# Kernel optimization log

Hardware: AMD Instinct MI355X
Metric: run time of the kernel (lower is better)

## Reference

```python
import jax, jax.numpy as jnp
import numpy as np

N_HEAD = 16
N_EMBD = 1024
BLOCK = 2048
B, T = 4, 2048


def setup_inputs() -> dict:
    key = jax.random.key(0)
    ks = jax.random.split(key, 5)
    s = 0.02
    return {
        "x": jax.random.normal(ks[0], (B, T, N_EMBD), dtype=jnp.float32),
        "qkv_w": jax.random.normal(ks[1], (3 * N_EMBD, N_EMBD), dtype=jnp.float32) * s,
        "qkv_b": jnp.zeros((3 * N_EMBD,), dtype=jnp.float32),
        "proj_w": jax.random.normal(ks[2], (N_EMBD, N_EMBD), dtype=jnp.float32) * s,
        "proj_b": jnp.zeros((N_EMBD,), dtype=jnp.float32),
    }


def reference(x, qkv_w, qkv_b, proj_w, proj_b):
    Bx, Tx, C = x.shape
    hd = C // N_HEAD
    qkv = x @ qkv_w.T + qkv_b  # [B,T,3C]
    q, k, v = jnp.split(qkv, 3, axis=-1)
    # [B,T,C] -> [B,H,T,hd]
    def heads(t):
        return t.reshape(Bx, Tx, N_HEAD, hd).transpose(0, 2, 1, 3)
    q, k, v = heads(q), heads(k), heads(v)
    scores = jnp.einsum("bhqd,bhkd->bhqk", q, k) / jnp.sqrt(jnp.float32(hd))
    causal = jnp.tril(jnp.ones((Tx, Tx), dtype=bool))
    scores = jnp.where(causal[None, None, :, :], scores, -jnp.inf)
    attn = jax.nn.softmax(scores, axis=-1)
    out = jnp.einsum("bhqk,bhkd->bhqd", attn, v)
    out = out.transpose(0, 2, 1, 3).reshape(Bx, Tx, C)
    return out @ proj_w.T + proj_b
```

## Files before the change

kernel.cpp:

```cpp
#include <hip/hip_runtime.h>
#include <stdint.h>
#include <math.h>

#define DEVI __device__ __forceinline__

typedef __attribute__((ext_vector_type(8))) short bf16x8;
typedef __attribute__((ext_vector_type(4))) float f32x4;

DEVI unsigned short f2bf(float f) {
  union { float f; unsigned u; } v; v.f = f;
  unsigned u = v.u;
  u += 0x7fffu + ((u >> 16) & 1u);
  return (unsigned short)(u >> 16);
}

DEVI unsigned cvt_pk_bf16(float a, float b) {
  unsigned r;
  asm("v_cvt_pk_bf16_f32 %0, %1, %2" : "=v"(r) : "v"(a), "v"(b));
  return r;
}

DEVI f32x4 mfma16(bf16x8 a, bf16x8 b, f32x4 c) {
  return __builtin_amdgcn_mfma_f32_16x16x32_bf16(a, b, c, 0, 0, 0);
}

DEVI void gld16(const unsigned short* g, unsigned short* l) {
  __builtin_amdgcn_global_load_lds(
      (const __attribute__((address_space(1))) unsigned int*)(uintptr_t)g,
      (__attribute__((address_space(3))) unsigned int*)(unsigned int)(uintptr_t)l,
      16, 0, 0);
}

#define VMCNT(n) asm volatile("s_waitcnt vmcnt(" #n ")" ::: "memory")
#define BAR()                              \
  do {                                     \
    __builtin_amdgcn_s_barrier();          \
    __builtin_amdgcn_sched_barrier(0);     \
  } while (0)
#define LBAR()                                              \
  do {                                                      \
    asm volatile("s_waitcnt lgkmcnt(0)" ::: "memory");      \
    __builtin_amdgcn_s_barrier();                           \
    __builtin_amdgcn_sched_barrier(0);                      \
  } while (0)

template <int N> DEVI void vmcntc() {
  static_assert(N >= 0 && N <= 8, "");
  if constexpr (N == 0) VMCNT(0);
  else if constexpr (N == 2) VMCNT(2);
  else if constexpr (N == 3) VMCNT(3);
  else if constexpr (N == 4) VMCNT(4);
}

__global__ __launch_bounds__(256) void cvt3_kernel(
    const float* __restrict__ a, unsigned short* __restrict__ oa,
    const float* __restrict__ b, unsigned short* __restrict__ ob,
    const float* __restrict__ c, unsigned short* __restrict__ oc) {
  int bid = blockIdx.x;
  const float* in; unsigned short* out; int i;
  if (bid < 4096)      { in = a; out = oa; i = bid; }
  else if (bid < 5632) { in = b; out = ob; i = bid - 4096; }
  else                 { in = c; out = oc; i = bid - 5632; }
  int idx = (i * 256 + (int)threadIdx.x) * 8;
#pragma unroll
  for (int u = 0; u < 2; ++u) {
    float4 v = *(const float4*)(in + idx + u * 4);
    uint2 o;
    o.x = cvt_pk_bf16(v.x, v.y);
    o.y = cvt_pk_bf16(v.z, v.w);
    *(uint2*)(out + idx + u * 4) = o;
  }
}

template <int MODE, int NTA, int NTB>
__global__ __launch_bounds__(512, 2) void gemm8(
    const unsigned short* __restrict__ A, const unsigned short* __restrict__ Bw,
    const float* __restrict__ bias, float* __restrict__ Cf,
    unsigned short* __restrict__ Qo, unsigned short* __restrict__ Ko,
    unsigned short* __restrict__ Vo, int M, int N, int K, int nbx) {
  constexpr int NTT = NTA + NTB;
  constexpr int WTN = NTT * 16;
  constexpr int BN = 4 * WTN;
  constexpr int B_USH = BN * 64;
  constexpr int BUFS = 16384 + B_USH;
  extern __shared__ unsigned short lds[];
  const int tid = threadIdx.x;
  const int lane = tid & 63;
  const int w = tid >> 6;
  const int wm = w >> 2, wn = w & 3;
  const int lr = lane & 15, lq = lane >> 4;

  const int cpx = gridDim.x >> 3;
  const int swz = (blockIdx.x & 7) * cpx + (blockIdx.x >> 3);
  const int bx = swz % nbx, by = swz / nbx;
  const int m0 = by * 256, n0 = bx * BN;

  const int sr = lane >> 3;
  const int sc = ((lane & 7) ^ sr) << 3;
  const unsigned short* pa = A + (size_t)(m0 + sr) * K + sc;
  const unsigned short* pb = Bw + (size_t)(n0 + sr) * K + sc;

  const int bs0 = (lq ^ (lr & 7)) << 3;
  const int bs1 = ((lq + 4) ^ (lr & 7)) << 3;

  f32x4 acc[8][NTT] = {};

  auto sA = [&](int buf, int kt, int c) {
    gld16(pa + (size_t)(c << 3) * K + kt, lds + buf * BUFS + (c << 9));
  };
  auto sB = [&](int buf, int kt, int c) {
    gld16(pb + (size_t)(c << 3) * K + kt, lds + buf * BUFS + 16384 + (c << 9));
  };
  auto sAa = [&](int buf, int kt) { sA(buf, kt, w); sA(buf, kt, 16 + w); };
  auto sAb = [&](int buf, int kt) { sA(buf, kt, 8 + w); sA(buf, kt, 24 + w); };
  auto sBa = [&](int buf, int kt) {
#pragma unroll
    for (int k2 = 0; k2 < NTA; ++k2)
      sB(buf, kt, (w & 3) * NTT * 2 + (w >> 2) * NTA + k2);
  };
  auto sBb = [&](int buf, int kt) {
#pragma unroll
    for (int k2 = 0; k2 < NTB; ++k2)
      sB(buf, kt, (w & 3) * NTT * 2 + NTA * 2 + (w >> 2) * NTB + k2);
  };

#define LDA(A_, mh)                                                          \
  _Pragma("unroll") for (int i = 0; i < 4; ++i) {                            \
    int ar = wm * 128 + (mh) * 64 + i * 16 + lr;                             \
    A_[i][0] = *(const bf16x8*)(As_ + ar * 64 + bs0);                        \
    A_[i][1] = *(const bf16x8*)(As_ + ar * 64 + bs1);                        \
  }
#define LDB(B_, CNT, ntb)                                                    \
  _Pragma("unroll") for (int j = 0; j < (CNT); ++j) {                        \
    int br = wn * WTN + ((ntb) + j) * 16 + lr;                               \
    B_[j][0] = *(const bf16x8*)(Bs_ + br * 64 + bs0);                        \
    B_[j][1] = *(const bf16x8*)(Bs_ + br * 64 + bs1);                        \
  }
#define MM(A_, B_, mh, CNT, ntb)                                             \
  __builtin_amdgcn_s_setprio(1);                                             \
  _Pragma("unroll") for (int i = 0; i < 4; ++i)                              \
    _Pragma("unroll") for (int j = 0; j < (CNT); ++j) {                      \
      acc[(mh) * 4 + i][(ntb) + j] =                                         \
          mfma16(A_[i][0], B_[j][0], acc[(mh) * 4 + i][(ntb) + j]);          \
      acc[(mh) * 4 + i][(ntb) + j] =                                         \
          mfma16(A_[i][1], B_[j][1], acc[(mh) * 4 + i][(ntb) + j]);          \
    }                                                                        \
  __builtin_amdgcn_s_setprio(0);

  sAa(0, 0); sBa(0, 0); sBb(0, 0); sAb(0, 0);
  vmcntc<NTB + 2>();
  BAR();

  const int NT = K >> 6;
  for (int t = 0; t < NT - 1; ++t) {
    const int buf = t & 1, nb = buf ^ 1;
    const int kt = (t + 1) << 6;
    const unsigned short* As_ = lds + buf * BUFS;
    const unsigned short* Bs_ = As_ + 16384;
    bf16x8 af[4][2], baf[NTA][2], bbf[NTB][2];
    sAa(nb, kt);
    LDA(af, 0); LDB(baf, NTA, 0);
    MM(af, baf, 0, NTA, 0);
    vmcntc<4>(); BAR();
    sBa(nb, kt);
    LDB(bbf, NTB, NTA);
    MM(af, bbf, 0, NTB, NTA);
    vmcntc<NTA + 2>(); BAR();
    sBb(nb, kt);
    LDA(af, 1);
    MM(af, bbf, 1, NTB, NTA);
    sAb(nb, kt);
    MM(af, baf, 1, NTA, 0);
    vmcntc<NTB + 2>(); BAR();
  }
  {
    const int buf = (NT - 1) & 1;
    const unsigned short* As_ = lds + buf * BUFS;
    const unsigned short* Bs_ = As_ + 16384;
    bf16x8 af[4][2], baf[NTA][2], bbf[NTB][2];
    LDA(af, 0); LDB(baf, NTA, 0);
    MM(af, baf, 0, NTA, 0);
    vmcntc<2>(); BAR();
    LDB(bbf, NTB, NTA);
    MM(af, bbf, 0, NTB, NTA);
    vmcntc<0>(); BAR();
    LDA(af, 1);
    MM(af, bbf, 1, NTB, NTA);
    MM(af, baf, 1, NTA, 0);
  }
#undef LDA
#undef LDB
#undef MM

#pragma unroll
  for (int mt = 0; mt < 8; ++mt) {
#pragma unroll
    for (int nt = 0; nt < NTT; ++nt) {
      int n_g = n0 + wn * WTN + nt * 16 + lr;
      float bv = bias[n_g];
      if (MODE == 1) {
#pragma unroll
        for (int r = 0; r < 4; ++r) {
          int m_g = m0 + wm * 128 + mt * 16 + lq * 4 + r;
          Cf[(size_t)m_g * N + n_g] = acc[mt][nt][r] + bv;
        }
      } else {
        int which = n_g >> 10;
        int rem = n_g & 1023;
        int h = rem >> 6, d = rem & 63;
        int m_base = m0 + wm * 128 + mt * 16 + lq * 4;
        int b = m_base >> 11, tt = m_base & 2047;
        if (which == 2) {
          uint2 pv;
          pv.x = cvt_pk_bf16(acc[mt][nt][0] + bv, acc[mt][nt][1] + bv);
          pv.y = cvt_pk_bf16(acc[mt][nt][2] + bv, acc[mt][nt][3] + bv);
          *(uint2*)(Vo + (((size_t)(b * 16 + h) * 64 + d) * 2048 + tt)) = pv;
        } else {
          unsigned short* p = (which == 0) ? Qo : Ko;
#pragma unroll
          for (int r = 0; r < 4; ++r) {
            size_t idx = (((size_t)(b * 16 + h) * 2048) + tt + r) * 64 + d;
            p[idx] = f2bf(acc[mt][nt][r] + bv);
          }
        }
      }
    }
  }
}

__global__ __launch_bounds__(512, 2) void attn_kernel(
    const unsigned short* __restrict__ Q, const unsigned short* __restrict__ K,
    const unsigned short* __restrict__ V, unsigned short* __restrict__ Y) {
  constexpr int T = 2048, HD = 64, H = 16;
  __shared__ unsigned short Kt[2][64 * 72];
  __shared__ unsigned short Vt[2][64 * 72];
  __shared__ unsigned short Pt[8][16 * 72];

  const int tid = threadIdx.x;
  const int lane = tid & 63;
  const int w = tid >> 6;
  const int lr = lane & 15, lq = lane >> 4;
  const int pair = blockIdx.x;
  const int h = blockIdx.y;
  const int b = blockIdx.z;
  const size_t bh = (size_t)(b * H + h) * T * HD;
  const float SC = 0.125f * 1.44269504089f;

  const int krow = tid >> 3, kcb = (tid & 7) << 3;

  float4 kr, vr;
  auto load_tile = [&](int jt) {
    const int c0 = jt * 64;
    kr = *(const float4*)(K + bh + (size_t)(c0 + krow) * HD + kcb);
    vr = *(const float4*)(V + bh + (size_t)krow * T + c0 + kcb);
  };
  auto stage = [&](int buf) {
    *(float4*)(&Kt[buf][krow * 72 + kcb]) = kr;
    *(float4*)(&Vt[buf][krow * 72 + kcb]) = vr;
  };

  load_tile(0);

  for (int phase = 0; phase < 2; ++phase) {
    const int qt = phase ? (7 - pair) : pair;
    const int q0 = qt * 256;
    const int nkv = 4 * (qt + 1);
    const int qw = q0 + w * 32;

    bf16x8 qf[2][2];
#pragma unroll
    for (int qs = 0; qs < 2; ++qs)
#pragma unroll
      for (int kb = 0; kb < 2; ++kb)
        qf[qs][kb] = *(const bf16x8*)(Q + bh + (size_t)(qw + qs * 16 + lr) * HD +
                                      kb * 32 + lq * 8);

    f32x4 o[2][4] = {};
    float mi[2] = {-INFINITY, -INFINITY}, li[2] = {0.f, 0.f};

    stage(0);
    load_tile(1);
    LBAR();

    for (int jt = 0; jt < nkv; ++jt) {
      const int c0 = jt * 64;
      const int buf = jt & 1;

      if (c0 <= qw + 31) {
        f32x4 s[2][4];
        __builtin_amdgcn_s_setprio(1);
#pragma unroll
        for (int nt = 0; nt < 4; ++nt) {
          bf16x8 kf0 = *(const bf16x8*)(&Kt[buf][(nt * 16 + lr) * 72 + lq * 8]);
          bf16x8 kf1 = *(const bf16x8*)(&Kt[buf][(nt * 16 + lr) * 72 + 32 + lq * 8]);
#pragma unroll
          for (int qs = 0; qs < 2; ++qs) {
            f32x4 z = {};
            z = mfma16(kf0, qf[qs][0], z);
            s[qs][nt] = mfma16(kf1, qf[qs][1], z);
          }
        }
        __builtin_amdgcn_s_setprio(0);
        if (c0 + 63 > qw) {
#pragma unroll
          for (int qs = 0; qs < 2; ++qs) {
            int qg = qw + qs * 16 + lr;
#pragma unroll
            for (int nt = 0; nt < 4; ++nt)
#pragma unroll
              for (int r = 0; r < 4; ++r) {
                int kvg = c0 + nt * 16 + lq * 4 + r;
                if (kvg > qg) s[qs][nt][r] = -INFINITY;
              }
          }
        }
        float mxs[2];
#pragma unroll
        for (int qs = 0; qs < 2; ++qs) {
          float mx = -INFINITY;
#pragma unroll
          for (int nt = 0; nt < 4; ++nt)
            mx = fmaxf(mx, fmaxf(fmaxf(s[qs][nt][0], s[qs][nt][1]),
                                 fmaxf(s[qs][nt][2], s[qs][nt][3])));
          mx = fmaxf(mx, __shfl_xor(mx, 16));
          mx = fmaxf(mx, __shfl_xor(mx, 32));
          mxs[qs] = mx * SC;
        }
        if (!__all((mxs[0] <= mi[0] + 8.f) && (mxs[1] <= mi[1] + 8.f))) {
#pragma unroll
          for (int qs = 0; qs < 2; ++qs) {
            float mnew = fmaxf(mi[qs], mxs[qs]);
            float alpha = __builtin_amdgcn_exp2f(mi[qs] - mnew);
            mi[qs] = mnew;
            li[qs] *= alpha;
#pragma unroll
            for (int nt = 0; nt < 4; ++nt)
#pragma unroll
              for (int r = 0; r < 4; ++r) o[qs][nt][r] *= alpha;
          }
        }
        bf16x8 pf[2][2];
#pragma unroll
        for (int qs = 0; qs < 2; ++qs) {
          float rs = 0.f;
#pragma unroll
          for (int nt = 0; nt < 4; ++nt) {
            float p0 = __builtin_amdgcn_exp2f(fmaf(s[qs][nt][0], SC, -mi[qs]));
            float p1 = __builtin_amdgcn_exp2f(fmaf(s[qs][nt][1], SC, -mi[qs]));
            float p2 = __builtin_amdgcn_exp2f(fmaf(s[qs][nt][2], SC, -mi[qs]));
            float p3 = __builtin_amdgcn_exp2f(fmaf(s[qs][nt][3], SC, -mi[qs]));
            rs += (p0 + p1) + (p2 + p3);
            uint2 pk;
            pk.x = cvt_pk_bf16(p0, p1);
            pk.y = cvt_pk_bf16(p2, p3);
            *(uint2*)(&Pt[w][lr * 72 + nt * 16 + lq * 4]) = pk;
          }
          li[qs] += rs;
#pragma unroll
          for (int kb = 0; kb < 2; ++kb)
            pf[qs][kb] = *(const bf16x8*)(&Pt[w][lr * 72 + kb * 32 + lq * 8]);
        }
        __builtin_amdgcn_s_setprio(1);
#pragma unroll
        for (int nt = 0; nt < 4; ++nt) {
          bf16x8 vf0 = *(const bf16x8*)(&Vt[buf][(nt * 16 + lr) * 72 + lq * 8]);
          bf16x8 vf1 = *(const bf16x8*)(&Vt[buf][(nt * 16 + lr) * 72 + 32 + lq * 8]);
#pragma unroll
          for (int qs = 0; qs < 2; ++qs) {
            o[qs][nt] = mfma16(vf0, pf[qs][0], o[qs][nt]);
            o[qs][nt] = mfma16(vf1, pf[qs][1], o[qs][nt]);
          }
        }
        __builtin_amdgcn_s_setprio(0);
      }

      if (jt + 1 < nkv) {
        stage(buf ^ 1);
        if (jt + 2 < nkv) load_tile(jt + 2);
        else if (phase == 0) load_tile(0);
        LBAR();
      }
    }

#pragma unroll
    for (int qs = 0; qs < 2; ++qs) {
      float l = li[qs];
      l += __shfl_xor(l, 16);
      l += __shfl_xor(l, 32);
      float inv = 1.f / l;
      int t_g = qw + qs * 16 + lr;
#pragma unroll
      for (int nt = 0; nt < 4; ++nt) {
        uint2 yv;
        yv.x = cvt_pk_bf16(o[qs][nt][0] * inv, o[qs][nt][1] * inv);
        yv.y = cvt_pk_bf16(o[qs][nt][2] * inv, o[qs][nt][3] * inv);
        *(uint2*)(Y + ((size_t)(b * T + t_g)) * 1024 + h * 64 + nt * 16 + lq * 4) = yv;
      }
    }
  }
}

extern "C" void kernel_launch(void* const* d_in, const int* in_sizes, int n_in,
                              void* d_out, int out_size, void* d_ws, size_t ws_size,
                              hipStream_t stream) {
  const float* x = (const float*)d_in[0];
  const float* qkv_w = (const float*)d_in[1];
  const float* qkv_b = (const float*)d_in[2];
  const float* proj_w = (const float*)d_in[3];
  const float* proj_b = (const float*)d_in[4];
  float* out = (float*)d_out;

  unsigned short* ws = (unsigned short*)d_ws;
  unsigned short* xb = ws;
  unsigned short* wqkv = xb + 8388608;
  unsigned short* wproj = wqkv + 3145728;
  unsigned short* Qb = wproj + 1048576;
  unsigned short* Kb = Qb + 8388608;
  unsigned short* Vb = Kb + 8388608;
  unsigned short* Yb = Vb + 8388608;

  auto* g0 = gemm8<0, 2, 1>;
  auto* g1 = gemm8<1, 1, 1>;
  static bool attr_set = false;
  if (!attr_set) {
    (void)hipFuncSetAttribute((const void*)g0,
                              hipFuncAttributeMaxDynamicSharedMemorySize, 114688);
    (void)hipFuncSetAttribute((const void*)g1,
                              hipFuncAttributeMaxDynamicSharedMemorySize, 98304);
    attr_set = true;
  }

  cvt3_kernel<<<6144, 256, 0, stream>>>(x, xb, qkv_w, wqkv, proj_w, wproj);

  gemm8<0, 2, 1><<<dim3(512), 512, 114688, stream>>>(xb, wqkv, qkv_b, nullptr, Qb,
                                                     Kb, Vb, 8192, 3072, 1024, 16);
  attn_kernel<<<dim3(4, 16, 4), 512, 0, stream>>>(Qb, Kb, Vb, Yb);
  gemm8<1, 1, 1><<<dim3(256), 512, 98304, stream>>>(Yb, wproj, proj_b, out, nullptr,
                                                    nullptr, nullptr, 8192, 1024,
                                                    1024, 8);
}
```

Baseline: 240.3 us.

## Parametrize GEMM M-tile, halve proj GEMM tile height; repad attention P buffer

Adds an MT template parameter so the GEMM block height can be 128 rows instead of 256. The output projection now uses this and launches 512 blocks instead of 256 with less LDS, aiming to fill more CUs on the smaller GEMM. Separately, the attention P scratch stride goes from 72 to 68 with split 8-byte reads, aiming to reduce LDS bank conflicts. Smaller tiles lower per-block data reuse, and the split reads add instructions.

```diff
diff --git a/kernel.cpp b/kernel.cpp
--- a/kernel.cpp
+++ b/kernel.cpp
@@ -47,6 +47,7 @@
 template <int N> DEVI void vmcntc() {
   static_assert(N >= 0 && N <= 8, "");
   if constexpr (N == 0) VMCNT(0);
+  else if constexpr (N == 1) VMCNT(1);
   else if constexpr (N == 2) VMCNT(2);
   else if constexpr (N == 3) VMCNT(3);
   else if constexpr (N == 4) VMCNT(4);
@@ -72,7 +73,7 @@
   }
 }
 
-template <int MODE, int NTA, int NTB>
+template <int MODE, int MT, int NTA, int NTB>
 __global__ __launch_bounds__(512, 2) void gemm8(
     const unsigned short* __restrict__ A, const unsigned short* __restrict__ Bw,
     const float* __restrict__ bias, float* __restrict__ Cf,
@@ -81,8 +82,11 @@
   constexpr int NTT = NTA + NTB;
   constexpr int WTN = NTT * 16;
   constexpr int BN = 4 * WTN;
+  constexpr int BM = MT * 32;
+  constexpr int AH = MT / 4;
+  constexpr int A_USH = BM * 64;
   constexpr int B_USH = BN * 64;
-  constexpr int BUFS = 16384 + B_USH;
+  constexpr int BUFS = A_USH + B_USH;
   extern __shared__ unsigned short lds[];
   const int tid = threadIdx.x;
   const int lane = tid & 63;
@@ -93,7 +97,7 @@
   const int cpx = gridDim.x >> 3;
   const int swz = (blockIdx.x & 7) * cpx + (blockIdx.x >> 3);
   const int bx = swz % nbx, by = swz / nbx;
-  const int m0 = by * 256, n0 = bx * BN;
+  const int m0 = by * BM, n0 = bx * BN;
 
   const int sr = lane >> 3;
   const int sc = ((lane & 7) ^ sr) << 3;
@@ -103,16 +107,24 @@
   const int bs0 = (lq ^ (lr & 7)) << 3;
   const int bs1 = ((lq + 4) ^ (lr & 7)) << 3;
 
-  f32x4 acc[8][NTT] = {};
+  f32x4 acc[MT][NTT] = {};
 
   auto sA = [&](int buf, int kt, int c) {
     gld16(pa + (size_t)(c << 3) * K + kt, lds + buf * BUFS + (c << 9));
   };
   auto sB = [&](int buf, int kt, int c) {
-    gld16(pb + (size_t)(c << 3) * K + kt, lds + buf * BUFS + 16384 + (c << 9));
-  };
-  auto sAa = [&](int buf, int kt) { sA(buf, kt, w); sA(buf, kt, 16 + w); };
-  auto sAb = [&](int buf, int kt) { sA(buf, kt, 8 + w); sA(buf, kt, 24 + w); };
+    gld16(pb + (size_t)(c << 3) * K + kt, lds + buf * BUFS + A_USH + (c << 9));
+  };
+  const int aA0 = (MT == 8) ? w : ((w & 3) + ((w >> 2) << 3));
+  const int aB0 = (MT == 8) ? (8 + w) : (aA0 + 4);
+  auto sAa = [&](int buf, int kt) {
+    sA(buf, kt, aA0);
+    if constexpr (MT == 8) sA(buf, kt, 16 + w);
+  };
+  auto sAb = [&](int buf, int kt) {
+    sA(buf, kt, aB0);
+    if constexpr (MT == 8) sA(buf, kt, 24 + w);
+  };
   auto sBa = [&](int buf, int kt) {
 #pragma unroll
     for (int k2 = 0; k2 < NTA; ++k2)
@@ -125,8 +137,8 @@
   };
 
 #define LDA(A_, mh)                                                          \
-  _Pragma("unroll") for (int i = 0; i < 4; ++i) {                            \
-    int ar = wm * 128 + (mh) * 64 + i * 16 + lr;                             \
+  _Pragma("unroll") for (int i = 0; i < MT / 2; ++i) {                       \
+    int ar = wm * (BM / 2) + (mh) * (BM / 4) + i * 16 + lr;                  \
     A_[i][0] = *(const bf16x8*)(As_ + ar * 64 + bs0);                        \
     A_[i][1] = *(const bf16x8*)(As_ + ar * 64 + bs1);                        \
   }
@@ -138,17 +150,17 @@
   }
 #define MM(A_, B_, mh, CNT, ntb)                                             \
   __builtin_amdgcn_s_setprio(1);                                             \
-  _Pragma("unroll") for (int i = 0; i < 4; ++i)                              \
+  _Pragma("unroll") for (int i = 0; i < MT / 2; ++i)                         \
     _Pragma("unroll") for (int j = 0; j < (CNT); ++j) {                      \
-      acc[(mh) * 4 + i][(ntb) + j] =                                         \
-          mfma16(A_[i][0], B_[j][0], acc[(mh) * 4 + i][(ntb) + j]);          \
-      acc[(mh) * 4 + i][(ntb) + j] =                                         \
-          mfma16(A_[i][1], B_[j][1], acc[(mh) * 4 + i][(ntb) + j]);          \
+      acc[(mh) * (MT / 2) + i][(ntb) + j] = mfma16(                          \
+          A_[i][0], B_[j][0], acc[(mh) * (MT / 2) + i][(ntb) + j]);          \
+      acc[(mh) * (MT / 2) + i][(ntb) + j] = mfma16(                          \
+          A_[i][1], B_[j][1], acc[(mh) * (MT / 2) + i][(ntb) + j]);          \
     }                                                                        \
   __builtin_amdgcn_s_setprio(0);
 
   sAa(0, 0); sBa(0, 0); sBb(0, 0); sAb(0, 0);
-  vmcntc<NTB + 2>();
+  vmcntc<NTB + AH>();
   BAR();
 
   const int NT = K >> 6;
@@ -156,31 +168,31 @@
     const int buf = t & 1, nb = buf ^ 1;
     const int kt = (t + 1) << 6;
     const unsigned short* As_ = lds + buf * BUFS;
-    const unsigned short* Bs_ = As_ + 16384;
-    bf16x8 af[4][2], baf[NTA][2], bbf[NTB][2];
+    const unsigned short* Bs_ = As_ + A_USH;
+    bf16x8 af[MT / 2][2], baf[NTA][2], bbf[NTB][2];
     sAa(nb, kt);
     LDA(af, 0); LDB(baf, NTA, 0);
     MM(af, baf, 0, NTA, 0);
-    vmcntc<4>(); BAR();
+    vmcntc<2 * AH>(); BAR();
     sBa(nb, kt);
     LDB(bbf, NTB, NTA);
     MM(af, bbf, 0, NTB, NTA);
-    vmcntc<NTA + 2>(); BAR();
+    vmcntc<AH + NTA>(); BAR();
     sBb(nb, kt);
     LDA(af, 1);
     MM(af, bbf, 1, NTB, NTA);
     sAb(nb, kt);
     MM(af, baf, 1, NTA, 0);
-    vmcntc<NTB + 2>(); BAR();
+    vmcntc<NTB + AH>(); BAR();
   }
   {
     const int buf = (NT - 1) & 1;
     const unsigned short* As_ = lds + buf * BUFS;
-    const unsigned short* Bs_ = As_ + 16384;
-    bf16x8 af[4][2], baf[NTA][2], bbf[NTB][2];
+    const unsigned short* Bs_ = As_ + A_USH;
+    bf16x8 af[MT / 2][2], baf[NTA][2], bbf[NTB][2];
     LDA(af, 0); LDB(baf, NTA, 0);
     MM(af, baf, 0, NTA, 0);
-    vmcntc<2>(); BAR();
+    vmcntc<AH>(); BAR();
     LDB(bbf, NTB, NTA);
     MM(af, bbf, 0, NTB, NTA);
     vmcntc<0>(); BAR();
@@ -193,7 +205,7 @@
 #undef MM
 
 #pragma unroll
-  for (int mt = 0; mt < 8; ++mt) {
+  for (int mt = 0; mt < MT; ++mt) {
 #pragma unroll
     for (int nt = 0; nt < NTT; ++nt) {
       int n_g = n0 + wn * WTN + nt * 16 + lr;
@@ -201,14 +213,14 @@
       if (MODE == 1) {
 #pragma unroll
         for (int r = 0; r < 4; ++r) {
-          int m_g = m0 + wm * 128 + mt * 16 + lq * 4 + r;
+          int m_g = m0 + wm * (BM / 2) + mt * 16 + lq * 4 + r;
           Cf[(size_t)m_g * N + n_g] = acc[mt][nt][r] + bv;
         }
       } else {
         int which = n_g >> 10;
         int rem = n_g & 1023;
         int h = rem >> 6, d = rem & 63;
-        int m_base = m0 + wm * 128 + mt * 16 + lq * 4;
+        int m_base = m0 + wm * (BM / 2) + mt * 16 + lq * 4;
         int b = m_base >> 11, tt = m_base & 2047;
         if (which == 2) {
           uint2 pv;
@@ -234,7 +246,7 @@
   constexpr int T = 2048, HD = 64, H = 16;
   __shared__ unsigned short Kt[2][64 * 72];
   __shared__ unsigned short Vt[2][64 * 72];
-  __shared__ unsigned short Pt[8][16 * 72];
+  __shared__ unsigned short Pt[8][16 * 68];
 
   const int tid = threadIdx.x;
   const int lane = tid & 63;
@@ -353,12 +365,17 @@
             uint2 pk;
             pk.x = cvt_pk_bf16(p0, p1);
             pk.y = cvt_pk_bf16(p2, p3);
-            *(uint2*)(&Pt[w][lr * 72 + nt * 16 + lq * 4]) = pk;
+            *(uint2*)(&Pt[w][lr * 68 + nt * 16 + lq * 4]) = pk;
           }
           li[qs] += rs;
 #pragma unroll
-          for (int kb = 0; kb < 2; ++kb)
-            pf[qs][kb] = *(const bf16x8*)(&Pt[w][lr * 72 + kb * 32 + lq * 8]);
+          for (int kb = 0; kb < 2; ++kb) {
+            union { uint2 u[2]; bf16x8 v; } pu;
+            pu.u[0] = *(const uint2*)(&Pt[w][lr * 68 + kb * 32 + lq * 8]);
+            __builtin_amdgcn_sched_barrier(0);
+            pu.u[1] = *(const uint2*)(&Pt[w][lr * 68 + kb * 32 + lq * 8 + 4]);
+            pf[qs][kb] = pu.v;
+          }
         }
         __builtin_amdgcn_s_setprio(1);
 #pragma unroll
@@ -419,23 +436,24 @@
   unsigned short* Vb = Kb + 8388608;
   unsigned short* Yb = Vb + 8388608;
 
-  auto* g0 = gemm8<0, 2, 1>;
-  auto* g1 = gemm8<1, 1, 1>;
+  auto* g0 = gemm8<0, 8, 2, 1>;
+  auto* g1 = gemm8<1, 4, 1, 1>;
   static bool attr_set = false;
   if (!attr_set) {
     (void)hipFuncSetAttribute((const void*)g0,
                               hipFuncAttributeMaxDynamicSharedMemorySize, 114688);
     (void)hipFuncSetAttribute((const void*)g1,
-                              hipFuncAttributeMaxDynamicSharedMemorySize, 98304);
+                              hipFuncAttributeMaxDynamicSharedMemorySize, 65536);
     attr_set = true;
   }
 
   cvt3_kernel<<<6144, 256, 0, stream>>>(x, xb, qkv_w, wqkv, proj_w, wproj);
 
-  gemm8<0, 2, 1><<<dim3(512), 512, 114688, stream>>>(xb, wqkv, qkv_b, nullptr, Qb,
-                                                     Kb, Vb, 8192, 3072, 1024, 16);
+  gemm8<0, 8, 2, 1><<<dim3(512), 512, 114688, stream>>>(xb, wqkv, qkv_b, nullptr,
+                                                        Qb, Kb, Vb, 8192, 3072,
+                                                        1024, 16);
   attn_kernel<<<dim3(4, 16, 4), 512, 0, stream>>>(Qb, Kb, Vb, Yb);
-  gemm8<1, 1, 1><<<dim3(256), 512, 98304, stream>>>(Yb, wproj, proj_b, out, nullptr,
-                                                    nullptr, nullptr, 8192, 1024,
-                                                    1024, 8);
-}
+  gemm8<1, 4, 1, 1><<<dim3(512), 512, 65536, stream>>>(Yb, wproj, proj_b, out,
+                                                       nullptr, nullptr, nullptr,
+                                                       8192, 1024, 1024, 8);
+}
```

After: 245.9 us. 2.3% more time.
